# Kernel tuning notes

Measured on AMD Instinct MI355X. Metric: run time of the kernel, lower is better.

Reference implementation:

```python
import jax, jax.numpy as jnp
import numpy as np

B, NT, NZ, CIN, H, DOUT, L = 16, 128, 256, 3, 64, 128, 3
N = NT * NZ  # 32768 nodes
EPS = 1e-5


def _build_edges():
    # Toroidal grid: each node connects to 4 neighbors (wrap-around in theta and zeta).
    T, Z = np.meshgrid(np.arange(NT), np.arange(NZ), indexing='ij')
    curr = (T * NZ + Z).ravel()
    nbrs = np.stack([
        (((T + 1) % NT) * NZ + Z).ravel(),
        (((T - 1) % NT) * NZ + Z).ravel(),
        (T * NZ + (Z + 1) % NZ).ravel(),
        (T * NZ + (Z - 1) % NZ).ravel(),
    ], axis=1)
    src = np.repeat(curr, 4)
    dst = nbrs.ravel()
    return np.stack([src, dst]).astype(np.int32)  # (2, 4N)


def setup_inputs() -> dict:
    key = jax.random.key(0)
    ks = jax.random.split(key, 8)
    s = lambda k, shp, fan: jax.random.normal(k, shp, jnp.float32) / np.float32(np.sqrt(fan))
    return {
        'x': jax.random.normal(ks[0], (B, CIN, N), jnp.float32),
        'edge_index': jnp.asarray(_build_edges()),
        'embed_W': s(ks[1], (CIN, H), CIN),
        'embed_b': jnp.zeros((H,), jnp.float32),
        'mp_W1': s(ks[2], (L, 2 * H, H), 2 * H),
        'mp_b1': jnp.zeros((L, H), jnp.float32),
        'mp_g1': jnp.ones((L, H), jnp.float32),
        'mp_be1': jnp.zeros((L, H), jnp.float32),
        'mp_W2': s(ks[3], (L, H, H), H),
        'mp_b2': jnp.zeros((L, H), jnp.float32),
        'mp_g2': jnp.ones((L, H), jnp.float32),
        'mp_be2': jnp.zeros((L, H), jnp.float32),
        'head_W1': s(ks[4], (H, H), H),
        'head_b1': jnp.zeros((H,), jnp.float32),
        'head_W2': s(ks[5], (H, DOUT), H),
        'head_b2': jnp.zeros((DOUT,), jnp.float32),
    }


def _bn(y, g, b):
    # BatchNorm1d in training mode: biased batch stats over (batch*nodes).
    m = y.mean(axis=(0, 1))
    v = y.var(axis=(0, 1))
    return (y - m) * (g * jax.lax.rsqrt(v + EPS)) + b


def reference(x, edge_index, embed_W, embed_b, mp_W1, mp_b1, mp_g1, mp_be1,
              mp_W2, mp_b2, mp_g2, mp_be2, head_W1, head_b1, head_W2, head_b2):
    src, dst = edge_index[0], edge_index[1]
    # embedding: (B,3,N) -> (B,N,H)
    h = jax.nn.relu(jnp.einsum('bcn,ch->bnh', x, embed_W) + embed_b)
    deg = jnp.zeros((N,), x.dtype).at[dst].add(1.0)
    deg = jnp.clip(deg, 1.0)[None, :, None]  # (1,N,1), all 4 on this graph
    for l in range(L):
        # gather neighbor features and scatter-add to destination, mean aggregate
        agg = jnp.zeros_like(h).at[:, dst, :].add(h[:, src, :]) / deg
        comb = jnp.concatenate([h, agg], axis=-1)  # (B,N,2H)
        y = jax.nn.relu(_bn(comb @ mp_W1[l] + mp_b1[l], mp_g1[l], mp_be1[l]))
        y = jax.nn.relu(_bn(y @ mp_W2[l] + mp_b2[l], mp_g2[l], mp_be2[l]))
        h = y + h  # residual (c_in == c_out)
    pooled = h.mean(axis=1)  # AdaptiveAvgPool1d(1) over nodes
    return jax.nn.relu(pooled @ head_W1 + head_b1) @ head_W2 + head_b2
```

## Files before the change

kernel.cpp:

```cpp
#include <hip/hip_runtime.h>

typedef unsigned short u16;
typedef u16 u16x8 __attribute__((ext_vector_type(8)));
typedef short s16x8 __attribute__((ext_vector_type(8)));
typedef float f32x4 __attribute__((ext_vector_type(4)));

#define NNODES 32768
#define EPSV 1e-5f
#define INV_ROWS (1.0f / 524288.0f)

__device__ __forceinline__ float bf2f(u16 u) {
  union { unsigned int i; float f; } v; v.i = ((unsigned int)u) << 16; return v.f;
}
__device__ __forceinline__ u16 f2bf(float f) {
  union { float f; unsigned int i; } v; v.f = f;
  unsigned int r = v.i + 0x7FFFu + ((v.i >> 16) & 1u);
  return (u16)(r >> 16);
}

__global__ __launch_bounds__(256) void k_embed(
    const float* __restrict__ x, const float* __restrict__ eW,
    const float* __restrict__ eb, u16* __restrict__ h) {
  int tid = threadIdx.x;
  int chunk = tid & 7;
  int r = blockIdx.x * 32 + (tid >> 3);
  int b = r >> 15;
  int n = r & 32767;
  const float* xb = x + (size_t)b * 3 * NNODES + n;
  float x0 = xb[0], x1 = xb[NNODES], x2 = xb[2 * NNODES];
  int c0 = chunk * 8;
  u16x8 ov;
#pragma unroll
  for (int j = 0; j < 8; ++j) {
    float acc = eb[c0 + j] + x0 * eW[c0 + j] + x1 * eW[64 + c0 + j] + x2 * eW[128 + c0 + j];
    ov[j] = f2bf(fmaxf(acc, 0.f));
  }
  *reinterpret_cast<u16x8*>(&h[(size_t)r * 64 + c0]) = ov;
}

__global__ __launch_bounds__(256) void k_gemm1(
    const u16* __restrict__ h, u16* __restrict__ ybuf,
    const float* __restrict__ W1, const float* __restrict__ b1,
    float* __restrict__ sums) {
  __shared__ __align__(16) u16 w_s[64 * 136];
  __shared__ __align__(16) u16 t_s[4][16 * 72];
  __shared__ float stat_s[4][128];

  int tid = threadIdx.x;
  int wv = tid >> 6, ln = tid & 63, ln15 = ln & 15, quad = ln >> 4;
  int blk = blockIdx.x;
  int xcd = blk & 7;
  int j = blk >> 3;
  int b = j >> 3;
  int local = j & 7;
  int tbase = (xcd * 8 + local) * 2;
  const u16* hb = h + (((size_t)b) << 15) * 64;

  for (int idx = tid; idx < 8192; idx += 256) {
    int k = idx >> 6, n = idx & 63;
    float w = W1[idx];
    if (k >= 64) w *= 0.25f;
    w_s[n * 136 + k] = f2bf(w);
  }
  __syncthreads();

  s16x8 bfT[4][2], bfB[4][2];
#pragma unroll
  for (int c = 0; c < 4; ++c)
#pragma unroll
    for (int kk = 0; kk < 2; ++kk) {
      bfT[c][kk] = *reinterpret_cast<const s16x8*>(
          &w_s[(c * 16 + ln15) * 136 + kk * 32 + quad * 8]);
      bfB[c][kk] = *reinterpret_cast<const s16x8*>(
          &w_s[(c * 16 + ln15) * 136 + 64 + kk * 32 + quad * 8]);
    }

  float bias_c[4];
#pragma unroll
  for (int c = 0; c < 4; ++c) bias_c[c] = b1[c * 16 + ln15];

  float ls[4] = {0.f, 0.f, 0.f, 0.f}, ls2[4] = {0.f, 0.f, 0.f, 0.f};
  u16* ts = &t_s[wv][0];
  int cA = quad * 8;

#pragma unroll 1
  for (int it = 0; it < 8; ++it) {
    int t = tbase + (it >> 2);
    int tp = (t + 1) & 127, tm = (t + 127) & 127;
    int z0 = (it & 3) * 64 + wv * 16;
    int z = z0 + ln15;
    int zp = (z + 1) & 255, zm = (z + 255) & 255;
    size_t rS  = ((size_t)(t * 256 + z)) * 64;
    size_t rTp = ((size_t)(tp * 256 + z)) * 64;
    size_t rTm = ((size_t)(tm * 256 + z)) * 64;
    size_t rZp = ((size_t)(t * 256 + zp)) * 64;
    size_t rZm = ((size_t)(t * 256 + zm)) * 64;

    s16x8 s0  = *reinterpret_cast<const s16x8*>(&hb[rS + cA]);
    s16x8 s1  = *reinterpret_cast<const s16x8*>(&hb[rS + 32 + cA]);
    s16x8 n0a = *reinterpret_cast<const s16x8*>(&hb[rTp + cA]);
    s16x8 n0b = *reinterpret_cast<const s16x8*>(&hb[rTp + 32 + cA]);
    s16x8 n1a = *reinterpret_cast<const s16x8*>(&hb[rTm + cA]);
    s16x8 n1b = *reinterpret_cast<const s16x8*>(&hb[rTm + 32 + cA]);
    s16x8 n2a = *reinterpret_cast<const s16x8*>(&hb[rZp + cA]);
    s16x8 n2b = *reinterpret_cast<const s16x8*>(&hb[rZp + 32 + cA]);
    s16x8 n3a = *reinterpret_cast<const s16x8*>(&hb[rZm + cA]);
    s16x8 n3b = *reinterpret_cast<const s16x8*>(&hb[rZm + 32 + cA]);

    f32x4 acc[4];
#pragma unroll
    for (int c = 0; c < 4; ++c) acc[c] = (f32x4){0.f, 0.f, 0.f, 0.f};
#pragma unroll
    for (int c = 0; c < 4; ++c) {
      acc[c] = __builtin_amdgcn_mfma_f32_16x16x32_bf16(s0,  bfT[c][0], acc[c], 0, 0, 0);
      acc[c] = __builtin_amdgcn_mfma_f32_16x16x32_bf16(s1,  bfT[c][1], acc[c], 0, 0, 0);
      acc[c] = __builtin_amdgcn_mfma_f32_16x16x32_bf16(n0a, bfB[c][0], acc[c], 0, 0, 0);
      acc[c] = __builtin_amdgcn_mfma_f32_16x16x32_bf16(n0b, bfB[c][1], acc[c], 0, 0, 0);
      acc[c] = __builtin_amdgcn_mfma_f32_16x16x32_bf16(n1a, bfB[c][0], acc[c], 0, 0, 0);
      acc[c] = __builtin_amdgcn_mfma_f32_16x16x32_bf16(n1b, bfB[c][1], acc[c], 0, 0, 0);
      acc[c] = __builtin_amdgcn_mfma_f32_16x16x32_bf16(n2a, bfB[c][0], acc[c], 0, 0, 0);
      acc[c] = __builtin_amdgcn_mfma_f32_16x16x32_bf16(n2b, bfB[c][1], acc[c], 0, 0, 0);
      acc[c] = __builtin_amdgcn_mfma_f32_16x16x32_bf16(n3a, bfB[c][0], acc[c], 0, 0, 0);
      acc[c] = __builtin_amdgcn_mfma_f32_16x16x32_bf16(n3b, bfB[c][1], acc[c], 0, 0, 0);
    }

    __builtin_amdgcn_wave_barrier();
#pragma unroll
    for (int c = 0; c < 4; ++c)
#pragma unroll
      for (int rg = 0; rg < 4; ++rg) {
        float vy = acc[c][rg] + bias_c[c];
        ls[c] += vy;
        ls2[c] += vy * vy;
        ts[(quad * 4 + rg) * 72 + c * 16 + ln15] = f2bf(vy);
      }
    __builtin_amdgcn_wave_barrier();
    size_t R0 = (((size_t)b) << 15) + (size_t)t * 256 + z0;
    int lr = ln >> 2;
#pragma unroll
    for (int p = 0; p < 2; ++p) {
      int ck = (ln & 3) + p * 4;
      u16x8 v = *reinterpret_cast<const u16x8*>(&ts[lr * 72 + ck * 8]);
      *reinterpret_cast<u16x8*>(&ybuf[(R0 + lr) * 64 + ck * 8]) = v;
    }
    __builtin_amdgcn_wave_barrier();
  }

#pragma unroll
  for (int c = 0; c < 4; ++c) {
    ls[c]  += __shfl_xor(ls[c], 16, 64);  ls[c]  += __shfl_xor(ls[c], 32, 64);
    ls2[c] += __shfl_xor(ls2[c], 16, 64); ls2[c] += __shfl_xor(ls2[c], 32, 64);
  }
  if (ln < 16) {
#pragma unroll
    for (int c = 0; c < 4; ++c) {
      stat_s[wv][c * 16 + ln] = ls[c];
      stat_s[wv][64 + c * 16 + ln] = ls2[c];
    }
  }
  __syncthreads();
  if (tid < 128) {
    float s = stat_s[0][tid] + stat_s[1][tid] + stat_s[2][tid] + stat_s[3][tid];
    atomicAdd(&sums[xcd * 128 + tid], s);
  }
}

__global__ __launch_bounds__(256) void k_gemm2(
    u16* __restrict__ ybuf, const float* __restrict__ W2,
    const float* __restrict__ b2, const float* __restrict__ sums1,
    const float* __restrict__ g1, const float* __restrict__ be1,
    float* __restrict__ sums2) {
  __shared__ __align__(16) u16 w_s[64 * 72];
  __shared__ __align__(16) u16 t_s[4][16 * 72];
  __shared__ float s1_s[64], sh1_s[64];
  __shared__ float stat_s[4][128];

  int tid = threadIdx.x;
  int wv = tid >> 6, ln = tid & 63, ln15 = ln & 15, quad = ln >> 4;

  if (tid < 64) {
    float s = 0.f, s2 = 0.f;
#pragma unroll
    for (int sl = 0; sl < 8; ++sl) { s += sums1[sl * 128 + tid]; s2 += sums1[sl * 128 + 64 + tid]; }
    float m = s * INV_ROWS;
    float v = s2 * INV_ROWS - m * m;
    float sc = g1[tid] * rsqrtf(v + EPSV);
    s1_s[tid] = sc;
    sh1_s[tid] = be1[tid] - m * sc;
  }
  for (int idx = tid; idx < 4096; idx += 256) {
    int k = idx >> 6, n = idx & 63;
    w_s[n * 72 + k] = f2bf(W2[idx]);
  }
  __syncthreads();

  s16x8 bf[4][2];
#pragma unroll
  for (int c = 0; c < 4; ++c)
#pragma unroll
    for (int kk = 0; kk < 2; ++kk)
      bf[c][kk] = *reinterpret_cast<const s16x8*>(
          &w_s[(c * 16 + ln15) * 72 + kk * 32 + quad * 8]);

  float sA[2][8], shA[2][8];
#pragma unroll
  for (int kk = 0; kk < 2; ++kk)
#pragma unroll
    for (int j = 0; j < 8; ++j) {
      int ch = kk * 32 + quad * 8 + j;
      sA[kk][j] = s1_s[ch];
      shA[kk][j] = sh1_s[ch];
    }

  float bias_c[4];
#pragma unroll
  for (int c = 0; c < 4; ++c) bias_c[c] = b2[c * 16 + ln15];

  float ls[4] = {0.f, 0.f, 0.f, 0.f}, ls2[4] = {0.f, 0.f, 0.f, 0.f};
  u16* ts = &t_s[wv][0];

#pragma unroll 1
  for (int it = 0; it < 8; ++it) {
    size_t r0 = (size_t)blockIdx.x * 512 + it * 64 + wv * 16;
    size_t row = r0 + ln15;
    u16x8 y0 = *reinterpret_cast<const u16x8*>(&ybuf[row * 64 + quad * 8]);
    u16x8 y1 = *reinterpret_cast<const u16x8*>(&ybuf[row * 64 + 32 + quad * 8]);
    s16x8 a0, a1;
#pragma unroll
    for (int j = 0; j < 8; ++j) {
      a0[j] = (short)f2bf(fmaxf(bf2f(y0[j]) * sA[0][j] + shA[0][j], 0.f));
      a1[j] = (short)f2bf(fmaxf(bf2f(y1[j]) * sA[1][j] + shA[1][j], 0.f));
    }

    f32x4 acc[4];
#pragma unroll
    for (int c = 0; c < 4; ++c) acc[c] = (f32x4){0.f, 0.f, 0.f, 0.f};
#pragma unroll
    for (int c = 0; c < 4; ++c) {
      acc[c] = __builtin_amdgcn_mfma_f32_16x16x32_bf16(a0, bf[c][0], acc[c], 0, 0, 0);
      acc[c] = __builtin_amdgcn_mfma_f32_16x16x32_bf16(a1, bf[c][1], acc[c], 0, 0, 0);
    }

    __builtin_amdgcn_wave_barrier();
#pragma unroll
    for (int c = 0; c < 4; ++c)
#pragma unroll
      for (int rg = 0; rg < 4; ++rg) {
        float vy = acc[c][rg] + bias_c[c];
        ls[c] += vy;
        ls2[c] += vy * vy;
        ts[(quad * 4 + rg) * 72 + c * 16 + ln15] = f2bf(vy);
      }
    __builtin_amdgcn_wave_barrier();
    int lr = ln >> 2;
#pragma unroll
    for (int p = 0; p < 2; ++p) {
      int ck = (ln & 3) + p * 4;
      u16x8 v = *reinterpret_cast<const u16x8*>(&ts[lr * 72 + ck * 8]);
      *reinterpret_cast<u16x8*>(&ybuf[(r0 + lr) * 64 + ck * 8]) = v;
    }
    __builtin_amdgcn_wave_barrier();
  }

#pragma unroll
  for (int c = 0; c < 4; ++c) {
    ls[c]  += __shfl_xor(ls[c], 16, 64);  ls[c]  += __shfl_xor(ls[c], 32, 64);
    ls2[c] += __shfl_xor(ls2[c], 16, 64); ls2[c] += __shfl_xor(ls2[c], 32, 64);
  }
  if (ln < 16) {
#pragma unroll
    for (int c = 0; c < 4; ++c) {
      stat_s[wv][c * 16 + ln] = ls[c];
      stat_s[wv][64 + c * 16 + ln] = ls2[c];
    }
  }
  __syncthreads();
  if (tid < 128) {
    float s = stat_s[0][tid] + stat_s[1][tid] + stat_s[2][tid] + stat_s[3][tid];
    atomicAdd(&sums2[(blockIdx.x & 7) * 128 + tid], s);
  }
}

__global__ __launch_bounds__(256) void k_resid(
    u16* __restrict__ h, const u16* __restrict__ zbuf,
    const float* __restrict__ sums2, const float* __restrict__ g2,
    const float* __restrict__ be2, float* __restrict__ pooled) {
  __shared__ float s2_s[64], sh2_s[64];
  __shared__ float red_s[32][68];
  int tid = threadIdx.x;
  if (tid < 64) {
    float s = 0.f, s2 = 0.f;
#pragma unroll
    for (int sl = 0; sl < 8; ++sl) { s += sums2[sl * 128 + tid]; s2 += sums2[sl * 128 + 64 + tid]; }
    float m = s * INV_ROWS;
    float v = s2 * INV_ROWS - m * m;
    float sc = g2[tid] * rsqrtf(v + EPSV);
    s2_s[tid] = sc;
    sh2_s[tid] = be2[tid] - m * sc;
  }
  __syncthreads();
  int ch0 = (tid & 7) * 8;
  float scl[8], shl[8];
#pragma unroll
  for (int j = 0; j < 8; ++j) { scl[j] = s2_s[ch0 + j]; shl[j] = sh2_s[ch0 + j]; }
  float p[8] = {0.f, 0.f, 0.f, 0.f, 0.f, 0.f, 0.f, 0.f};
  size_t base0 = (size_t)blockIdx.x * 16384 + tid * 8;
#pragma unroll 1
  for (int it = 0; it < 8; ++it) {
    size_t base = base0 + it * 2048;
    u16x8 zv = *reinterpret_cast<const u16x8*>(&zbuf[base]);
    u16x8 hv = *reinterpret_cast<const u16x8*>(&h[base]);
    u16x8 ov;
#pragma unroll
    for (int j = 0; j < 8; ++j) {
      float a = fmaxf(bf2f(zv[j]) * scl[j] + shl[j], 0.f);
      float nh = bf2f(hv[j]) + a;
      ov[j] = f2bf(nh);
      p[j] += bf2f(ov[j]);
    }
    *reinterpret_cast<u16x8*>(&h[base]) = ov;
  }
  if (pooled != nullptr) {
    int g = tid >> 3;
#pragma unroll
    for (int j = 0; j < 8; ++j) red_s[g][ch0 + j] = p[j];
    __syncthreads();
    if (tid < 64) {
      float s = 0.f;
#pragma unroll
      for (int gg = 0; gg < 32; ++gg) s += red_s[gg][tid];
      atomicAdd(&pooled[(blockIdx.x >> 7) * 64 + tid], s);
    }
  }
}

__global__ __launch_bounds__(256) void k_head(
    const float* __restrict__ pooled, const float* __restrict__ hW1,
    const float* __restrict__ hb1, const float* __restrict__ hW2,
    const float* __restrict__ hb2, float* __restrict__ out) {
  __shared__ float p_s[16 * 64];
  __shared__ float t1_s[16 * 64];
  int tid = threadIdx.x;
#pragma unroll
  for (int j = 0; j < 4; ++j)
    p_s[tid + 256 * j] = pooled[tid + 256 * j] * (1.0f / 32768.0f);
  __syncthreads();
#pragma unroll
  for (int j = 0; j < 4; ++j) {
    int idx = tid + 256 * j;
    int bb = idx >> 6, o = idx & 63;
    float acc = hb1[o];
    for (int k = 0; k < 64; ++k) acc += p_s[bb * 64 + k] * hW1[k * 64 + o];
    t1_s[idx] = fmaxf(acc, 0.f);
  }
  __syncthreads();
#pragma unroll
  for (int j = 0; j < 8; ++j) {
    int idx = tid + 256 * j;
    int bb = idx >> 7, o = idx & 127;
    float acc = hb2[o];
    for (int k = 0; k < 64; ++k) acc += t1_s[bb * 64 + k] * hW2[k * 128 + o];
    out[idx] = acc;
  }
}

extern "C" void kernel_launch(void* const* d_in, const int* in_sizes, int n_in,
                              void* d_out, int out_size, void* d_ws, size_t ws_size,
                              hipStream_t stream) {
  const float* x   = (const float*)d_in[0];
  const float* eW  = (const float*)d_in[2];
  const float* eb  = (const float*)d_in[3];
  const float* W1  = (const float*)d_in[4];
  const float* b1  = (const float*)d_in[5];
  const float* g1  = (const float*)d_in[6];
  const float* be1 = (const float*)d_in[7];
  const float* W2  = (const float*)d_in[8];
  const float* b2  = (const float*)d_in[9];
  const float* g2  = (const float*)d_in[10];
  const float* be2 = (const float*)d_in[11];
  const float* hW1 = (const float*)d_in[12];
  const float* hb1 = (const float*)d_in[13];
  const float* hW2 = (const float*)d_in[14];
  const float* hb2 = (const float*)d_in[15];
  float* out = (float*)d_out;

  char* ws = (char*)d_ws;
  u16* h    = (u16*)ws;
  u16* ybuf = (u16*)(ws + 67108864);
  float* stats  = (float*)(ws + 134217728);
  float* pooled = stats + 6144;

  hipMemsetAsync(stats, 0, (6144 + 1024) * sizeof(float), stream);

  k_embed<<<16384, 256, 0, stream>>>(x, eW, eb, h);
  for (int l = 0; l < 3; ++l) {
    float* sum1 = stats + l * 2048;
    float* sum2 = stats + l * 2048 + 1024;
    k_gemm1<<<1024, 256, 0, stream>>>(h, ybuf, W1 + l * 8192, b1 + l * 64, sum1);
    k_gemm2<<<1024, 256, 0, stream>>>(ybuf, W2 + l * 4096, b2 + l * 64,
                                      sum1, g1 + l * 64, be1 + l * 64, sum2);
    k_resid<<<2048, 256, 0, stream>>>(h, ybuf, sum2, g2 + l * 64, be2 + l * 64,
                                      (l == 2) ? pooled : nullptr);
  }
  k_head<<<1, 256, 0, stream>>>(pooled, hW1, hb1, hW2, hb2, out);
}
```

Before: 489.7 us.

## Pre-convert weights once, load MFMA fragments from global, double grid size

```diff
diff --git a/kernel.cpp b/kernel.cpp
--- a/kernel.cpp
+++ b/kernel.cpp
@@ -16,6 +16,26 @@
   union { float f; unsigned int i; } v; v.f = f;
   unsigned int r = v.i + 0x7FFFu + ((v.i >> 16) & 1u);
   return (u16)(r >> 16);
+}
+
+__global__ __launch_bounds__(256) void k_prep(
+    const float* __restrict__ W1, const float* __restrict__ W2,
+    u16* __restrict__ w1t, u16* __restrict__ w2t) {
+  int idx = blockIdx.x * 256 + threadIdx.x;
+  if (idx < 24576) {
+    int l = idx >> 13, rem = idx & 8191;
+    int n = rem >> 7, k = rem & 127;
+    float w = W1[l * 8192 + k * 64 + n];
+    if (k >= 64) w *= 0.25f;
+    w1t[idx] = f2bf(w);
+  } else {
+    int idx2 = idx - 24576;
+    if (idx2 < 12288) {
+      int l = idx2 >> 12, rem = idx2 & 4095;
+      int n = rem >> 6, k = rem & 63;
+      w2t[idx2] = f2bf(W2[l * 4096 + k * 64 + n]);
+    }
+  }
 }
 
 __global__ __launch_bounds__(256) void k_embed(
@@ -40,9 +60,8 @@
 
 __global__ __launch_bounds__(256) void k_gemm1(
     const u16* __restrict__ h, u16* __restrict__ ybuf,
-    const float* __restrict__ W1, const float* __restrict__ b1,
+    const u16* __restrict__ w1t, const float* __restrict__ b1,
     float* __restrict__ sums) {
-  __shared__ __align__(16) u16 w_s[64 * 136];
   __shared__ __align__(16) u16 t_s[4][16 * 72];
   __shared__ float stat_s[4][128];
 
@@ -51,18 +70,10 @@
   int blk = blockIdx.x;
   int xcd = blk & 7;
   int j = blk >> 3;
-  int b = j >> 3;
-  int local = j & 7;
-  int tbase = (xcd * 8 + local) * 2;
+  int b = j >> 4;
+  int t = xcd * 16 + (j & 15);
   const u16* hb = h + (((size_t)b) << 15) * 64;
-
-  for (int idx = tid; idx < 8192; idx += 256) {
-    int k = idx >> 6, n = idx & 63;
-    float w = W1[idx];
-    if (k >= 64) w *= 0.25f;
-    w_s[n * 136 + k] = f2bf(w);
-  }
-  __syncthreads();
+  int tp = (t + 1) & 127, tm = (t + 127) & 127;
 
   s16x8 bfT[4][2], bfB[4][2];
 #pragma unroll
@@ -70,9 +81,9 @@
 #pragma unroll
     for (int kk = 0; kk < 2; ++kk) {
       bfT[c][kk] = *reinterpret_cast<const s16x8*>(
-          &w_s[(c * 16 + ln15) * 136 + kk * 32 + quad * 8]);
+          &w1t[(c * 16 + ln15) * 128 + kk * 32 + quad * 8]);
       bfB[c][kk] = *reinterpret_cast<const s16x8*>(
-          &w_s[(c * 16 + ln15) * 136 + 64 + kk * 32 + quad * 8]);
+          &w1t[(c * 16 + ln15) * 128 + 64 + kk * 32 + quad * 8]);
     }
 
   float bias_c[4];
@@ -84,10 +95,8 @@
   int cA = quad * 8;
 
 #pragma unroll 1
-  for (int it = 0; it < 8; ++it) {
-    int t = tbase + (it >> 2);
-    int tp = (t + 1) & 127, tm = (t + 127) & 127;
-    int z0 = (it & 3) * 64 + wv * 16;
+  for (int st = 0; st < 4; ++st) {
+    int z0 = st * 64 + wv * 16;
     int z = z0 + ln15;
     int zp = (z + 1) & 255, zm = (z + 255) & 255;
     size_t rS  = ((size_t)(t * 256 + z)) * 64;
@@ -166,11 +175,10 @@
 }
 
 __global__ __launch_bounds__(256) void k_gemm2(
-    u16* __restrict__ ybuf, const float* __restrict__ W2,
+    u16* __restrict__ ybuf, const u16* __restrict__ w2t,
     const float* __restrict__ b2, const float* __restrict__ sums1,
     const float* __restrict__ g1, const float* __restrict__ be1,
     float* __restrict__ sums2) {
-  __shared__ __align__(16) u16 w_s[64 * 72];
   __shared__ __align__(16) u16 t_s[4][16 * 72];
   __shared__ float s1_s[64], sh1_s[64];
   __shared__ float stat_s[4][128];
@@ -188,11 +196,6 @@
     s1_s[tid] = sc;
     sh1_s[tid] = be1[tid] - m * sc;
   }
-  for (int idx = tid; idx < 4096; idx += 256) {
-    int k = idx >> 6, n = idx & 63;
-    w_s[n * 72 + k] = f2bf(W2[idx]);
-  }
-  __syncthreads();
 
   s16x8 bf[4][2];
 #pragma unroll
@@ -200,7 +203,13 @@
 #pragma unroll
     for (int kk = 0; kk < 2; ++kk)
       bf[c][kk] = *reinterpret_cast<const s16x8*>(
-          &w_s[(c * 16 + ln15) * 72 + kk * 32 + quad * 8]);
+          &w2t[(c * 16 + ln15) * 64 + kk * 32 + quad * 8]);
+
+  float bias_c[4];
+#pragma unroll
+  for (int c = 0; c < 4; ++c) bias_c[c] = b2[c * 16 + ln15];
+
+  __syncthreads();
 
   float sA[2][8], shA[2][8];
 #pragma unroll
@@ -212,16 +221,12 @@
       shA[kk][j] = sh1_s[ch];
     }
 
-  float bias_c[4];
-#pragma unroll
-  for (int c = 0; c < 4; ++c) bias_c[c] = b2[c * 16 + ln15];
-
   float ls[4] = {0.f, 0.f, 0.f, 0.f}, ls2[4] = {0.f, 0.f, 0.f, 0.f};
   u16* ts = &t_s[wv][0];
 
 #pragma unroll 1
-  for (int it = 0; it < 8; ++it) {
-    size_t r0 = (size_t)blockIdx.x * 512 + it * 64 + wv * 16;
+  for (int st = 0; st < 4; ++st) {
+    size_t r0 = (size_t)blockIdx.x * 256 + st * 64 + wv * 16;
     size_t row = r0 + ln15;
     u16x8 y0 = *reinterpret_cast<const u16x8*>(&ybuf[row * 64 + quad * 8]);
     u16x8 y1 = *reinterpret_cast<const u16x8*>(&ybuf[row * 64 + 32 + quad * 8]);
@@ -306,19 +311,30 @@
   float p[8] = {0.f, 0.f, 0.f, 0.f, 0.f, 0.f, 0.f, 0.f};
   size_t base0 = (size_t)blockIdx.x * 16384 + tid * 8;
 #pragma unroll 1
-  for (int it = 0; it < 8; ++it) {
-    size_t base = base0 + it * 2048;
-    u16x8 zv = *reinterpret_cast<const u16x8*>(&zbuf[base]);
-    u16x8 hv = *reinterpret_cast<const u16x8*>(&h[base]);
-    u16x8 ov;
+  for (int it = 0; it < 8; it += 2) {
+    size_t ba = base0 + it * 2048;
+    size_t bb = ba + 2048;
+    u16x8 zva = *reinterpret_cast<const u16x8*>(&zbuf[ba]);
+    u16x8 hva = *reinterpret_cast<const u16x8*>(&h[ba]);
+    u16x8 zvb = *reinterpret_cast<const u16x8*>(&zbuf[bb]);
+    u16x8 hvb = *reinterpret_cast<const u16x8*>(&h[bb]);
+    u16x8 ova, ovb;
 #pragma unroll
     for (int j = 0; j < 8; ++j) {
-      float a = fmaxf(bf2f(zv[j]) * scl[j] + shl[j], 0.f);
-      float nh = bf2f(hv[j]) + a;
-      ov[j] = f2bf(nh);
-      p[j] += bf2f(ov[j]);
-    }
-    *reinterpret_cast<u16x8*>(&h[base]) = ov;
+      float a = fmaxf(bf2f(zva[j]) * scl[j] + shl[j], 0.f);
+      float nh = bf2f(hva[j]) + a;
+      ova[j] = f2bf(nh);
+      p[j] += bf2f(ova[j]);
+    }
+    *reinterpret_cast<u16x8*>(&h[ba]) = ova;
+#pragma unroll
+    for (int j = 0; j < 8; ++j) {
+      float a = fmaxf(bf2f(zvb[j]) * scl[j] + shl[j], 0.f);
+      float nh = bf2f(hvb[j]) + a;
+      ovb[j] = f2bf(nh);
+      p[j] += bf2f(ovb[j]);
+    }
+    *reinterpret_cast<u16x8*>(&h[bb]) = ovb;
   }
   if (pooled != nullptr) {
     int g = tid >> 3;
@@ -389,15 +405,18 @@
   u16* ybuf = (u16*)(ws + 67108864);
   float* stats  = (float*)(ws + 134217728);
   float* pooled = stats + 6144;
+  u16* w1t = (u16*)(ws + 134217728 + 7168 * 4);
+  u16* w2t = w1t + 24576;
 
   hipMemsetAsync(stats, 0, (6144 + 1024) * sizeof(float), stream);
 
+  k_prep<<<144, 256, 0, stream>>>(W1, W2, w1t, w2t);
   k_embed<<<16384, 256, 0, stream>>>(x, eW, eb, h);
   for (int l = 0; l < 3; ++l) {
     float* sum1 = stats + l * 2048;
     float* sum2 = stats + l * 2048 + 1024;
-    k_gemm1<<<1024, 256, 0, stream>>>(h, ybuf, W1 + l * 8192, b1 + l * 64, sum1);
-    k_gemm2<<<1024, 256, 0, stream>>>(ybuf, W2 + l * 4096, b2 + l * 64,
+    k_gemm1<<<2048, 256, 0, stream>>>(h, ybuf, w1t + l * 8192, b1 + l * 64, sum1);
+    k_gemm2<<<2048, 256, 0, stream>>>(ybuf, w2t + l * 4096, b2 + l * 64,
                                       sum1, g1 + l * 64, be1 + l * 64, sum2);
     k_resid<<<2048, 256, 0, stream>>>(h, ybuf, sum2, g2 + l * 64, be2 + l * 64,
                                       (l == 2) ? pooled : nullptr);
```

Result: no change. 484.6 us (-1.0%).
